# Optimization experiments

Measured on AMD Instinct MI355X. Metric: run time of the kernel, lower is better.

## Reference

```python
import jax, jax.numpy as jnp
import numpy as np

N, L, C, H = 8, 2048, 512, 512
C_HALF = max(C // 2, 1)


def setup_inputs() -> dict:
    key = jax.random.key(0)
    ks = jax.random.split(key, 11)
    s = 0.02
    return {
        "x": jax.random.normal(ks[0], (N, L, C), dtype=jnp.float32),
        "theta_w": jax.random.normal(ks[1], (C, H), dtype=jnp.float32) * s,
        "theta_b": jax.random.normal(ks[2], (H,), dtype=jnp.float32) * s,
        "phi_w": jax.random.normal(ks[3], (C, H), dtype=jnp.float32) * s,
        "phi_b": jax.random.normal(ks[4], (H,), dtype=jnp.float32) * s,
        "psi_w": jax.random.normal(ks[5], (C, H), dtype=jnp.float32) * s,
        "psi_b": jax.random.normal(ks[6], (H,), dtype=jnp.float32) * s,
        "r1_w": jax.random.normal(ks[7], (H, C_HALF), dtype=jnp.float32) * s,
        "r1_b": jax.random.normal(ks[8], (C_HALF,), dtype=jnp.float32) * s,
        "r2_w": jax.random.normal(ks[9], (C_HALF, C), dtype=jnp.float32) * s,
        "r2_b": jax.random.normal(ks[10], (C,), dtype=jnp.float32) * s,
    }


def reference(x, theta_w, theta_b, phi_w, phi_b, psi_w, psi_b, r1_w, r1_b, r2_w, r2_b):
    # projections: [n, L, h]
    x_t = x @ theta_w + theta_b
    x_ph = x @ phi_w + phi_b
    x_psi = x @ psi_w + psi_b
    # unscaled attention: phi @ theta^T -> [n, L, L], softmax over last dim
    attn = jax.nn.softmax(jnp.einsum("nlh,nmh->nlm", x_ph, x_t), axis=2)
    x_add = jnp.einsum("nlm,nmh->nlh", attn, x_psi)
    # recover MLP with LeakyReLU(0.2) then Tanh, residual add
    h1 = jax.nn.leaky_relu(x_add @ r1_w + r1_b, negative_slope=0.2)
    h2 = jnp.tanh(h1 @ r2_w + r2_b)
    return x + h2
```

## Files before the change

### kernel.cpp

```cpp
#include <hip/hip_runtime.h>
#include <hip/hip_bf16.h>

typedef float f32x4 __attribute__((ext_vector_type(4)));
typedef int   v8i   __attribute__((ext_vector_type(8)));
typedef __attribute__((address_space(3))) unsigned int       lds_uint;
typedef __attribute__((address_space(1))) const unsigned int glb_uint;

__device__ __forceinline__ float tanh_fast(float x) {
    float e = __expf(-2.0f * fabsf(x));
    float r = (1.0f - e) / (1.0f + e);
    return copysignf(r, x);
}
__device__ __forceinline__ unsigned char f2fp8(float v) {
    return (unsigned char)(__builtin_amdgcn_cvt_pk_fp8_f32(v, 0.0f, 0, false) & 0xff);
}
__device__ __forceinline__ unsigned short f2h(float v) {
    _Float16 h = (_Float16)v;
    unsigned short u;
    __builtin_memcpy(&u, &h, 2);
    return u;
}
__device__ __forceinline__ float h2f(unsigned short u) {
    _Float16 h;
    __builtin_memcpy(&h, &u, 2);
    return (float)h;
}

__global__ __launch_bounds__(256) void prep(
    const float* __restrict__ x,
    const float* __restrict__ theta_w, const float* __restrict__ phi_w,
    const float* __restrict__ psi_w,   const float* __restrict__ r1_w,
    const float* __restrict__ r2_w,
    const float* __restrict__ theta_b, const float* __restrict__ phi_b,
    const float* __restrict__ psi_b,
    unsigned char* __restrict__ xb8, unsigned char* __restrict__ wCat8T,
    unsigned char* __restrict__ r1T8, unsigned char* __restrict__ r2T8,
    float* __restrict__ bCat) {
    const int b = blockIdx.x, t = threadIdx.x;
    if (b < 8192) {
        long i = ((long)b * 256 + t) * 4;
        float4 f = *(const float4*)(x + i);
        int w = __builtin_amdgcn_cvt_pk_fp8_f32(f.x, f.y, 0, false);
        w = __builtin_amdgcn_cvt_pk_fp8_f32(f.z, f.w, w, true);
        *(unsigned int*)(xb8 + i) = (unsigned int)w;
    } else if (b < 11264) {
        const int sel = (b - 8192) >> 10;
        const int idx = ((b - 8192) & 1023) * 256 + t;
        const float* w = sel == 0 ? theta_w : (sel == 1 ? phi_w : psi_w);
        const int r = idx >> 9, c = idx & 511;
        wCat8T[(long)(sel * 512 + c) * 512 + r] = f2fp8(w[idx] * 16.0f);
    } else if (b < 11776) {
        const int idx = (b - 11264) * 256 + t;
        const int r = idx >> 8, c = idx & 255;
        r1T8[(long)c * 512 + r] = f2fp8(r1_w[idx] * 16.0f);
    } else if (b < 12288) {
        const int idx = (b - 11776) * 256 + t;
        const int r = idx >> 9, c = idx & 511;
        r2T8[(long)c * 256 + r] = f2fp8(r2_w[idx] * 16.0f);
    } else {
        const int i = (b - 12288) * 256 + t;
        if (i < 1536)
            bCat[i] = i < 512 ? theta_b[i] : (i < 1024 ? phi_b[i - 512] : psi_b[i - 1024]);
    }
}

__global__ __launch_bounds__(256) void softmax_fp8(unsigned short* __restrict__ S) {
    const size_t row = (size_t)blockIdx.y * 2048 + blockIdx.x;
    unsigned short* p = S + row * 2048;
    const int t = threadIdx.x;
    uint4 raw = *(uint4*)(p + t * 8);
    unsigned int w[4] = {raw.x, raw.y, raw.z, raw.w};
    float v[8];
#pragma unroll
    for (int i = 0; i < 4; ++i) {
        v[2 * i]     = h2f((unsigned short)(w[i] & 0xffffu));
        v[2 * i + 1] = h2f((unsigned short)(w[i] >> 16));
    }
    float mx = v[0];
#pragma unroll
    for (int i = 1; i < 8; ++i) mx = fmaxf(mx, v[i]);
#pragma unroll
    for (int off = 32; off > 0; off >>= 1) mx = fmaxf(mx, __shfl_xor(mx, off));
    __shared__ float red[8];
    const int wave = t >> 6, lane = t & 63;
    if (lane == 0) red[wave] = mx;
    __syncthreads();
    mx = fmaxf(fmaxf(red[0], red[1]), fmaxf(red[2], red[3]));
    float s = 0.0f;
#pragma unroll
    for (int i = 0; i < 8; ++i) { v[i] = __expf(v[i] - mx); s += v[i]; }
#pragma unroll
    for (int off = 32; off > 0; off >>= 1) s += __shfl_xor(s, off);
    if (lane == 0) red[4 + wave] = s;
    __syncthreads();
    s = red[4] + red[5] + red[6] + red[7];
    const float inv = 1.0f / s;
    int o0 = __builtin_amdgcn_cvt_pk_fp8_f32(v[0] * inv, v[1] * inv, 0, false);
    o0 = __builtin_amdgcn_cvt_pk_fp8_f32(v[2] * inv, v[3] * inv, o0, true);
    int o1 = __builtin_amdgcn_cvt_pk_fp8_f32(v[4] * inv, v[5] * inv, 0, false);
    o1 = __builtin_amdgcn_cvt_pk_fp8_f32(v[6] * inv, v[7] * inv, o1, true);
    uint2 ov; ov.x = (unsigned int)o0; ov.y = (unsigned int)o1;
    *(uint2*)((unsigned char*)p + t * 8) = ov;
}

template <int MODE>
__global__ __launch_bounds__(256) void gemm_fp8(
    const unsigned char* __restrict__ A,
    const unsigned char* __restrict__ Bt,
    const float* __restrict__ bias,
    const float* __restrict__ resid,
    unsigned char* __restrict__ out8,
    float* __restrict__ outF,
    int K, int ldaB, int ldbB, int ldc, long sA, long sB, long sC) {
    __shared__ unsigned char As[2][128 * 128];
    __shared__ unsigned char Bs[2][128 * 128];

    const int tid  = threadIdx.x;
    const int lane = tid & 63, wave = tid >> 6;
    const int m16  = lane & 15, quad = lane >> 4;
    const int wm   = (wave >> 1) << 6, wn = (wave & 1) << 6;
    const int m0   = blockIdx.x << 7, n0 = blockIdx.y << 7;

    const int srow = lane >> 3;
    const int uswz = (lane & 7) ^ srow;

    const unsigned char* Abase = A  + (long)blockIdx.z * sA + (long)m0 * ldaB;
    const unsigned char* Bbase = Bt + (long)blockIdx.z * sB + (long)n0 * ldbB;
    const int stR = (wave << 5) + srow;
    const long gA0 = (long)stR * ldaB + (uswz << 4);
    const long gB0 = (long)stR * ldbB + (uswz << 4);

    const int s8  = m16 & 7;
    const int P   = quad ^ (s8 >> 1);
    const int cLo = (P << 1) + (s8 & 1);
    const int offLo = cLo << 4;
    const int offHi = (cLo ^ 1) << 4;

    f32x4 acc[4][4] = {};
    union F8 { v8i v; int4 q[2]; };

    auto STAGE = [&](int buf, int kk) {
#pragma unroll
        for (int i = 0; i < 4; ++i) {
            const unsigned char* gp = Abase + gA0 + (long)(i << 3) * ldaB + kk;
            unsigned char* lp = &As[buf][((wave << 5) + (i << 3)) << 7];
            __builtin_amdgcn_global_load_lds((glb_uint*)gp, (lds_uint*)lp, 16, 0, 0);
        }
#pragma unroll
        for (int i = 0; i < 4; ++i) {
            const unsigned char* gp = Bbase + gB0 + (long)(i << 3) * ldbB + kk;
            unsigned char* lp = &Bs[buf][((wave << 5) + (i << 3)) << 7];
            __builtin_amdgcn_global_load_lds((glb_uint*)gp, (lds_uint*)lp, 16, 0, 0);
        }
    };

    STAGE(0, 0);
    int cur = 0;
    for (int k0 = 0; k0 < K; k0 += 128) {
        if (k0 + 128 < K) {
            STAGE(cur ^ 1, k0 + 128);
            asm volatile("s_waitcnt vmcnt(8)" ::: "memory");
        } else {
            asm volatile("s_waitcnt vmcnt(0)" ::: "memory");
        }
        asm volatile("s_barrier" ::: "memory");

        const unsigned char* Ab = As[cur];
        const unsigned char* Bb = Bs[cur];
        F8 af[4], bg[4];
#pragma unroll
        for (int f = 0; f < 4; ++f) {
            const int m = wm + (f << 4) + m16;
            const int n = wn + (f << 4) + m16;
            af[f].q[0] = *(const int4*)&Ab[(m << 7) + offLo];
            af[f].q[1] = *(const int4*)&Ab[(m << 7) + offHi];
            bg[f].q[0] = *(const int4*)&Bb[(n << 7) + offLo];
            bg[f].q[1] = *(const int4*)&Bb[(n << 7) + offHi];
        }
#pragma unroll
        for (int fi = 0; fi < 4; ++fi)
#pragma unroll
            for (int fj = 0; fj < 4; ++fj)
                acc[fi][fj] = __builtin_amdgcn_mfma_scale_f32_16x16x128_f8f6f4(
                    af[fi].v, bg[fj].v, acc[fi][fj],
                    0, 0, 0, 127, 0, 127);

        asm volatile("s_waitcnt lgkmcnt(0)" ::: "memory");
        asm volatile("s_barrier" ::: "memory");
        cur ^= 1;
    }

    const long zC = (long)blockIdx.z * sC;

#pragma unroll
    for (int fj = 0; fj < 4; ++fj) {
        const int col = n0 + wn + (fj << 4) + m16;
        float bv = 0.0f;
        if (MODE >= 3) bv = bias[col];
#pragma unroll
        for (int fi = 0; fi < 4; ++fi)
#pragma unroll
            for (int r = 0; r < 4; ++r) {
                const int row = m0 + wm + (fi << 4) + (quad << 2) + r;
                float v = acc[fi][fj][r];
                if (MODE == 2) {
                    out8[zC + (long)row * 512 + col] = f2fp8(v);
                } else if (MODE == 3) {
                    v = v * 0.0625f + bv;
                    v = v > 0.0f ? v : 0.2f * v;
                    out8[(long)row * 256 + col] = f2fp8(v);
                } else {
                    v = v * 0.0625f + bv;
                    const long idx = (long)row * ldc + col;
                    outF[idx] = tanh_fast(v) + resid[idx];
                }
            }
    }
}

template <int MODE>
__global__ __launch_bounds__(512, 2) void gemm_fp8_big(
    const unsigned char* __restrict__ A,
    const unsigned char* __restrict__ Bt,
    const float* __restrict__ bias,
    unsigned short* __restrict__ outH,
    unsigned char* __restrict__ out8,
    unsigned char* __restrict__ out8b,
    unsigned char* __restrict__ outV,
    int K, int ldaB, int ldbB, int ldc, long sA, long sB, long sC) {
    __shared__ unsigned char As[2][256 * 128];
    __shared__ unsigned char Bs[2][256 * 128];

    const int tid  = threadIdx.x;
    const int lane = tid & 63, wave = tid >> 6;
    const int m16  = lane & 15, quad = lane >> 4;
    const int wm   = (wave >> 2) << 7;
    const int wn   = (wave & 3) << 6;
    const int m0   = blockIdx.x << 8, n0 = blockIdx.y << 8;

    const int srow = lane >> 3;
    const int uswz = (lane & 7) ^ srow;

    const unsigned char* Abase = A  + (long)blockIdx.z * sA + (long)m0 * ldaB;
    const unsigned char* Bbase = Bt + (long)blockIdx.z * sB + (long)n0 * ldbB;
    const int stR = (wave << 5) + srow;
    const long gA0 = (long)stR * ldaB + (uswz << 4);
    const long gB0 = (long)stR * ldbB + (uswz << 4);

    const int s8  = m16 & 7;
    const int P   = quad ^ (s8 >> 1);
    const int cLo = (P << 1) + (s8 & 1);
    const int offLo = cLo << 4;
    const int offHi = (cLo ^ 1) << 4;

    f32x4 acc[8][4] = {};
    union F8 { v8i v; int4 q[2]; };

    auto STAGE = [&](int buf, int kk) {
#pragma unroll
        for (int i = 0; i < 4; ++i) {
            const unsigned char* gp = Abase + gA0 + (long)(i << 3) * ldaB + kk;
            unsigned char* lp = &As[buf][((wave << 5) + (i << 3)) << 7];
            __builtin_amdgcn_global_load_lds((glb_uint*)gp, (lds_uint*)lp, 16, 0, 0);
        }
#pragma unroll
        for (int i = 0; i < 4; ++i) {
            const unsigned char* gp = Bbase + gB0 + (long)(i << 3) * ldbB + kk;
            unsigned char* lp = &Bs[buf][((wave << 5) + (i << 3)) << 7];
            __builtin_amdgcn_global_load_lds((glb_uint*)gp, (lds_uint*)lp, 16, 0, 0);
        }
    };

    STAGE(0, 0);
    int cur = 0;
    for (int k0 = 0; k0 < K; k0 += 128) {
        if (k0 + 128 < K) {
            STAGE(cur ^ 1, k0 + 128);
            asm volatile("s_waitcnt vmcnt(8)" ::: "memory");
        } else {
            asm volatile("s_waitcnt vmcnt(0)" ::: "memory");
        }
        asm volatile("s_barrier" ::: "memory");

        const unsigned char* Ab = As[cur];
        const unsigned char* Bb = Bs[cur];
        F8 bg[4];
#pragma unroll
        for (int fj = 0; fj < 4; ++fj) {
            const int n = wn + (fj << 4) + m16;
            bg[fj].q[0] = *(const int4*)&Bb[(n << 7) + offLo];
            bg[fj].q[1] = *(const int4*)&Bb[(n << 7) + offHi];
        }
#pragma unroll
        for (int fi = 0; fi < 8; ++fi) {
            F8 af;
            const int m = wm + (fi << 4) + m16;
            af.q[0] = *(const int4*)&Ab[(m << 7) + offLo];
            af.q[1] = *(const int4*)&Ab[(m << 7) + offHi];
#pragma unroll
            for (int fj = 0; fj < 4; ++fj)
                acc[fi][fj] = __builtin_amdgcn_mfma_scale_f32_16x16x128_f8f6f4(
                    af.v, bg[fj].v, acc[fi][fj],
                    0, 0, 0, 127, 0, 127);
        }

        asm volatile("s_waitcnt lgkmcnt(0)" ::: "memory");
        asm volatile("s_barrier" ::: "memory");
        cur ^= 1;
    }

    const long zC = (long)blockIdx.z * sC;

    if (MODE == 0) {
        const int sel = n0 >> 9;
        if (sel < 2) {
            unsigned char* dst = sel == 0 ? out8 : out8b;
#pragma unroll
            for (int fj = 0; fj < 4; ++fj) {
                const int col = n0 + wn + (fj << 4) + m16;
                const int cb  = col & 511;
                const float bv = bias[col];
#pragma unroll
                for (int fi = 0; fi < 8; ++fi)
#pragma unroll
                    for (int r = 0; r < 4; ++r) {
                        const int row = m0 + wm + (fi << 4) + (quad << 2) + r;
                        dst[(long)row * 512 + cb] = f2fp8(acc[fi][fj][r] * 0.0625f + bv);
                    }
            }
        } else {
            const int z = m0 >> 11, l0 = (m0 & 2047) + wm + (quad << 2);
#pragma unroll
            for (int fj = 0; fj < 4; ++fj) {
                const int col = n0 + wn + (fj << 4) + m16;
                const int h   = col & 511;
                const float bv = bias[col];
#pragma unroll
                for (int fi = 0; fi < 8; ++fi) {
                    int w = __builtin_amdgcn_cvt_pk_fp8_f32(
                        acc[fi][fj][0] * 0.0625f + bv, acc[fi][fj][1] * 0.0625f + bv, 0, false);
                    w = __builtin_amdgcn_cvt_pk_fp8_f32(
                        acc[fi][fj][2] * 0.0625f + bv, acc[fi][fj][3] * 0.0625f + bv, w, true);
                    *(unsigned int*)(outV + ((long)z * 512 + h) * 2048 + l0 + (fi << 4)) =
                        (unsigned int)w;
                }
            }
        }
    } else {
#pragma unroll
        for (int fj = 0; fj < 4; ++fj) {
            const int col = n0 + wn + (fj << 4) + m16;
#pragma unroll
            for (int fi = 0; fi < 8; ++fi)
#pragma unroll
                for (int r = 0; r < 4; ++r) {
                    const int row = m0 + wm + (fi << 4) + (quad << 2) + r;
                    outH[zC + (long)row * ldc + col] = f2h(acc[fi][fj][r]);
                }
        }
    }
}

extern "C" void kernel_launch(void* const* d_in, const int* in_sizes, int n_in,
                              void* d_out, int out_size, void* d_ws, size_t ws_size,
                              hipStream_t stream) {
    const float* x       = (const float*)d_in[0];
    const float* theta_w = (const float*)d_in[1];
    const float* theta_b = (const float*)d_in[2];
    const float* phi_w   = (const float*)d_in[3];
    const float* phi_b   = (const float*)d_in[4];
    const float* psi_w   = (const float*)d_in[5];
    const float* psi_b   = (const float*)d_in[6];
    const float* r1_w    = (const float*)d_in[7];
    const float* r1_b    = (const float*)d_in[8];
    const float* r2_w    = (const float*)d_in[9];
    const float* r2_b    = (const float*)d_in[10];
    float* out = (float*)d_out;

    constexpr int  N = 8, L = 2048, C = 512, H = 512, CH = 256;
    constexpr long NL = (long)N * L;

    char* p = (char*)d_ws;
    auto alloc = [&](size_t bytes) { void* q = (void*)p; p += bytes; return q; };
    unsigned char*  xb8    = (unsigned char*)alloc(NL * C);
    unsigned char*  TH8    = (unsigned char*)alloc(NL * H);
    unsigned char*  PH8    = (unsigned char*)alloc(NL * H);
    unsigned char*  VT8    = (unsigned char*)alloc((long)N * H * L);
    unsigned char*  xadd8  = (unsigned char*)alloc(NL * H);
    unsigned char*  h18    = (unsigned char*)alloc(NL * CH);
    unsigned char*  wCat8T = (unsigned char*)alloc((long)1536 * 512);
    unsigned char*  r1T8   = (unsigned char*)alloc((long)H * CH);
    unsigned char*  r2T8   = (unsigned char*)alloc((long)CH * C);
    float*          bCat   = (float*)alloc(1536 * 4 + 256);
    unsigned short* S      = (unsigned short*)alloc((long)N * L * L * 2);

    prep<<<12294, 256, 0, stream>>>(x, theta_w, phi_w, psi_w, r1_w, r2_w,
                                    theta_b, phi_b, psi_b, xb8, wCat8T, r1T8, r2T8, bCat);

    gemm_fp8_big<0><<<dim3(NL / 256, 1536 / 256, 1), 512, 0, stream>>>(
        xb8, wCat8T, bCat, nullptr, TH8, PH8, VT8,
        C, C, C, 0, 0, 0, 0);

    gemm_fp8_big<1><<<dim3(L / 256, L / 256, N), 512, 0, stream>>>(
        PH8, TH8, nullptr, S, nullptr, nullptr, nullptr,
        H, H, H, L, (long)L * H, (long)L * H, (long)L * L);

    softmax_fp8<<<dim3(L, N), 256, 0, stream>>>(S);

    gemm_fp8<2><<<dim3(L / 128, H / 128, N), 256, 0, stream>>>(
        (const unsigned char*)S, VT8, nullptr, nullptr, xadd8, nullptr,
        L, 2 * L, L, H, (long)L * 2 * L, (long)H * L, (long)L * H);

    gemm_fp8<3><<<dim3(NL / 128, CH / 128, 1), 256, 0, stream>>>(
        xadd8, r1T8, r1_b, nullptr, h18, nullptr,
        H, H, H, CH, 0, 0, 0);

    gemm_fp8<4><<<dim3(NL / 128, C / 128, 1), 256, 0, stream>>>(
        h18, r2T8, r2_b, x, nullptr, out,
        CH, CH, CH, C, 0, 0, 0);
}
```

Baseline: 227.9 us.

## Rewrite 256-tile fp8 GEMM with quarter-staged prefetch and batch-interleaved block order

Replaces the big fp8 GEMM with a version that issues the next K-tile's loads in four quarters interleaved with four compute phases, each phase loading two A fragments, with barriers between phases and s_setprio raised around the MFMA groups. It also flattens the grid for the batched S and attention-V GEMMs so consecutive block IDs map to different batch indices, which changes how blocks are spread across XCDs and caches. Launch bounds drop the min-2-blocks hint. The goal is better overlap of global-to-LDS traffic with MFMA work. The cost is extra barriers per K-step and possibly more register pressure without the occupancy hint.

```diff
diff --git a/kernel.cpp b/kernel.cpp
--- a/kernel.cpp
+++ b/kernel.cpp
@@ -104,6 +104,161 @@
 }
 
 template <int MODE>
+__global__ __launch_bounds__(512) void gemm256(
+    const unsigned char* __restrict__ A,
+    const unsigned char* __restrict__ Bt,
+    const float* __restrict__ bias,
+    unsigned short* __restrict__ outH,
+    unsigned char* __restrict__ out8,
+    unsigned char* __restrict__ out8b,
+    unsigned char* __restrict__ outV,
+    int K, int ldaB, int ldbB, int ldc, long sA, long sB, long sC) {
+    __shared__ unsigned char As[2][256 * 128];
+    __shared__ unsigned char Bs[2][256 * 128];
+
+    const int tid  = threadIdx.x;
+    const int lane = tid & 63, wave = tid >> 6;
+    const int m16  = lane & 15, quad = lane >> 4;
+    const int wm   = (wave >> 2) << 7;
+    const int wn   = (wave & 3) << 6;
+
+    int bx, by, z;
+    if constexpr (MODE == 1) {
+        z = blockIdx.x & 7;
+        const int t = blockIdx.x >> 3;
+        by = t & 7; bx = t >> 3;
+    } else {
+        bx = blockIdx.x; by = blockIdx.y; z = 0;
+    }
+    const int m0 = bx << 8, n0 = by << 8;
+
+    const unsigned char* Abase = A  + (long)z * sA + (long)m0 * ldaB;
+    const unsigned char* Bbase = Bt + (long)z * sB + (long)n0 * ldbB;
+
+    const int s8  = m16 & 7;
+    const int P   = quad ^ (s8 >> 1);
+    const int cLo = (P << 1) + (s8 & 1);
+    const int offLo = cLo << 4;
+    const int offHi = (cLo ^ 1) << 4;
+
+    f32x4 acc[8][4] = {};
+    union F8 { v8i v; int4 q[2]; };
+
+    auto STAGEQ = [&](int buf, int kk, int q) {
+        const bool isA = !(q & 1);
+        const int  h   = q >> 1;
+        const unsigned char* gb = isA ? Abase : Bbase;
+        const long ld = isA ? (long)ldaB : (long)ldbB;
+        unsigned char* lb = isA ? As[buf] : Bs[buf];
+#pragma unroll
+        for (int i = 0; i < 2; ++i) {
+            const int slot = wave * 2 + i;
+            const int row  = h * 128 + slot * 8 + (lane >> 3);
+            const int su   = (lane & 7) ^ (row & 7);
+            __builtin_amdgcn_global_load_lds(
+                (glb_uint*)(gb + (long)row * ld + kk + (su << 4)),
+                (lds_uint*)(lb + h * 16384 + slot * 1024), 16, 0, 0);
+        }
+    };
+
+    const int KT = K >> 7;
+    STAGEQ(0, 0, 0); STAGEQ(0, 0, 1); STAGEQ(0, 0, 2); STAGEQ(0, 0, 3);
+
+    for (int t = 0; t < KT; ++t) {
+        const int  cb  = t & 1;
+        const int  kk1 = (t + 1) << 7;
+        const bool pf  = (t + 1 < KT);
+        F8 bg[4];
+#pragma unroll
+        for (int p = 0; p < 4; ++p) {
+            if (pf) STAGEQ(cb ^ 1, kk1, p);
+            if (p == 0) {
+                if (pf) asm volatile("s_waitcnt vmcnt(2)" ::: "memory");
+                else    asm volatile("s_waitcnt vmcnt(0)" ::: "memory");
+            }
+            asm volatile("s_barrier" ::: "memory");
+
+            F8 af[2];
+            if (p == 0) {
+#pragma unroll
+                for (int fj = 0; fj < 4; ++fj) {
+                    const int n = wn + (fj << 4) + m16;
+                    bg[fj].q[0] = *(const int4*)&Bs[cb][(n << 7) + offLo];
+                    bg[fj].q[1] = *(const int4*)&Bs[cb][(n << 7) + offHi];
+                }
+            }
+#pragma unroll
+            for (int e = 0; e < 2; ++e) {
+                const int m = wm + (((p << 1) + e) << 4) + m16;
+                af[e].q[0] = *(const int4*)&As[cb][(m << 7) + offLo];
+                af[e].q[1] = *(const int4*)&As[cb][(m << 7) + offHi];
+            }
+            asm volatile("s_waitcnt lgkmcnt(0)" ::: "memory");
+            __builtin_amdgcn_s_setprio(1);
+#pragma unroll
+            for (int e = 0; e < 2; ++e)
+#pragma unroll
+                for (int fj = 0; fj < 4; ++fj)
+                    acc[(p << 1) + e][fj] = __builtin_amdgcn_mfma_scale_f32_16x16x128_f8f6f4(
+                        af[e].v, bg[fj].v, acc[(p << 1) + e][fj], 0, 0, 0, 127, 0, 127);
+            __builtin_amdgcn_s_setprio(0);
+            asm volatile("s_barrier" ::: "memory");
+        }
+    }
+
+    if (MODE == 0) {
+        const int sel = n0 >> 9;
+        if (sel < 2) {
+            unsigned char* dst = sel == 0 ? out8 : out8b;
+#pragma unroll
+            for (int fj = 0; fj < 4; ++fj) {
+                const int col = n0 + wn + (fj << 4) + m16;
+                const int cb2 = col & 511;
+                const float bv = bias[col];
+#pragma unroll
+                for (int fi = 0; fi < 8; ++fi)
+#pragma unroll
+                    for (int r = 0; r < 4; ++r) {
+                        const int row = m0 + wm + (fi << 4) + (quad << 2) + r;
+                        dst[(long)row * 512 + cb2] = f2fp8(acc[fi][fj][r] * 0.0625f + bv);
+                    }
+            }
+        } else {
+            const int zz = m0 >> 11;
+#pragma unroll
+            for (int fj = 0; fj < 4; ++fj) {
+                const int col = n0 + wn + (fj << 4) + m16;
+                const int h   = col & 511;
+                const float bv = bias[col];
+#pragma unroll
+                for (int fi = 0; fi < 8; ++fi) {
+                    const int l0v = (m0 & 2047) + wm + (fi << 4) + (quad << 2);
+                    int w = __builtin_amdgcn_cvt_pk_fp8_f32(
+                        acc[fi][fj][0] * 0.0625f + bv, acc[fi][fj][1] * 0.0625f + bv, 0, false);
+                    w = __builtin_amdgcn_cvt_pk_fp8_f32(
+                        acc[fi][fj][2] * 0.0625f + bv, acc[fi][fj][3] * 0.0625f + bv, w, true);
+                    *(unsigned int*)(outV + ((long)zz * 512 + h) * 2048 + l0v) =
+                        (unsigned int)w;
+                }
+            }
+        }
+    } else {
+        const long zC = (long)z * sC;
+#pragma unroll
+        for (int fj = 0; fj < 4; ++fj) {
+            const int col = n0 + wn + (fj << 4) + m16;
+#pragma unroll
+            for (int fi = 0; fi < 8; ++fi)
+#pragma unroll
+                for (int r = 0; r < 4; ++r) {
+                    const int row = m0 + wm + (fi << 4) + (quad << 2) + r;
+                    outH[zC + (long)row * ldc + col] = f2h(acc[fi][fj][r]);
+                }
+        }
+    }
+}
+
+template <int MODE>
 __global__ __launch_bounds__(256) void gemm_fp8(
     const unsigned char* __restrict__ A,
     const unsigned char* __restrict__ Bt,
@@ -119,13 +274,22 @@
     const int lane = tid & 63, wave = tid >> 6;
     const int m16  = lane & 15, quad = lane >> 4;
     const int wm   = (wave >> 1) << 6, wn = (wave & 1) << 6;
-    const int m0   = blockIdx.x << 7, n0 = blockIdx.y << 7;
+
+    int bx, by, z;
+    if constexpr (MODE == 2) {
+        z = blockIdx.x & 7;
+        const int t = blockIdx.x >> 3;
+        by = t & 3;  bx = t >> 2;
+    } else {
+        bx = blockIdx.x; by = blockIdx.y; z = 0;
+    }
+    const int m0 = bx << 7, n0 = by << 7;
 
     const int srow = lane >> 3;
     const int uswz = (lane & 7) ^ srow;
 
-    const unsigned char* Abase = A  + (long)blockIdx.z * sA + (long)m0 * ldaB;
-    const unsigned char* Bbase = Bt + (long)blockIdx.z * sB + (long)n0 * ldbB;
+    const unsigned char* Abase = A  + (long)z * sA + (long)m0 * ldaB;
+    const unsigned char* Bbase = Bt + (long)z * sB + (long)n0 * ldbB;
     const int stR = (wave << 5) + srow;
     const long gA0 = (long)stR * ldaB + (uswz << 4);
     const long gB0 = (long)stR * ldbB + (uswz << 4);
@@ -190,7 +354,7 @@
         cur ^= 1;
     }
 
-    const long zC = (long)blockIdx.z * sC;
+    const long zC = (long)z * sC;
 
 #pragma unroll
     for (int fj = 0; fj < 4; ++fj) {
@@ -215,149 +379,6 @@
                     outF[idx] = tanh_fast(v) + resid[idx];
                 }
             }
-    }
-}
-
-template <int MODE>
-__global__ __launch_bounds__(512, 2) void gemm_fp8_big(
-    const unsigned char* __restrict__ A,
-    const unsigned char* __restrict__ Bt,
-    const float* __restrict__ bias,
-    unsigned short* __restrict__ outH,
-    unsigned char* __restrict__ out8,
-    unsigned char* __restrict__ out8b,
-    unsigned char* __restrict__ outV,
-    int K, int ldaB, int ldbB, int ldc, long sA, long sB, long sC) {
-    __shared__ unsigned char As[2][256 * 128];
-    __shared__ unsigned char Bs[2][256 * 128];
-
-    const int tid  = threadIdx.x;
-    const int lane = tid & 63, wave = tid >> 6;
-    const int m16  = lane & 15, quad = lane >> 4;
-    const int wm   = (wave >> 2) << 7;
-    const int wn   = (wave & 3) << 6;
-    const int m0   = blockIdx.x << 8, n0 = blockIdx.y << 8;
-
-    const int srow = lane >> 3;
-    const int uswz = (lane & 7) ^ srow;
-
-    const unsigned char* Abase = A  + (long)blockIdx.z * sA + (long)m0 * ldaB;
-    const unsigned char* Bbase = Bt + (long)blockIdx.z * sB + (long)n0 * ldbB;
-    const int stR = (wave << 5) + srow;
-    const long gA0 = (long)stR * ldaB + (uswz << 4);
-    const long gB0 = (long)stR * ldbB + (uswz << 4);
-
-    const int s8  = m16 & 7;
-    const int P   = quad ^ (s8 >> 1);
-    const int cLo = (P << 1) + (s8 & 1);
-    const int offLo = cLo << 4;
-    const int offHi = (cLo ^ 1) << 4;
-
-    f32x4 acc[8][4] = {};
-    union F8 { v8i v; int4 q[2]; };
-
-    auto STAGE = [&](int buf, int kk) {
-#pragma unroll
-        for (int i = 0; i < 4; ++i) {
-            const unsigned char* gp = Abase + gA0 + (long)(i << 3) * ldaB + kk;
-            unsigned char* lp = &As[buf][((wave << 5) + (i << 3)) << 7];
-            __builtin_amdgcn_global_load_lds((glb_uint*)gp, (lds_uint*)lp, 16, 0, 0);
-        }
-#pragma unroll
-        for (int i = 0; i < 4; ++i) {
-            const unsigned char* gp = Bbase + gB0 + (long)(i << 3) * ldbB + kk;
-            unsigned char* lp = &Bs[buf][((wave << 5) + (i << 3)) << 7];
-            __builtin_amdgcn_global_load_lds((glb_uint*)gp, (lds_uint*)lp, 16, 0, 0);
-        }
-    };
-
-    STAGE(0, 0);
-    int cur = 0;
-    for (int k0 = 0; k0 < K; k0 += 128) {
-        if (k0 + 128 < K) {
-            STAGE(cur ^ 1, k0 + 128);
-            asm volatile("s_waitcnt vmcnt(8)" ::: "memory");
-        } else {
-            asm volatile("s_waitcnt vmcnt(0)" ::: "memory");
-        }
-        asm volatile("s_barrier" ::: "memory");
-
-        const unsigned char* Ab = As[cur];
-        const unsigned char* Bb = Bs[cur];
-        F8 bg[4];
-#pragma unroll
-        for (int fj = 0; fj < 4; ++fj) {
-            const int n = wn + (fj << 4) + m16;
-            bg[fj].q[0] = *(const int4*)&Bb[(n << 7) + offLo];
-            bg[fj].q[1] = *(const int4*)&Bb[(n << 7) + offHi];
-        }
-#pragma unroll
-        for (int fi = 0; fi < 8; ++fi) {
-            F8 af;
-            const int m = wm + (fi << 4) + m16;
-            af.q[0] = *(const int4*)&Ab[(m << 7) + offLo];
-            af.q[1] = *(const int4*)&Ab[(m << 7) + offHi];
-#pragma unroll
-            for (int fj = 0; fj < 4; ++fj)
-                acc[fi][fj] = __builtin_amdgcn_mfma_scale_f32_16x16x128_f8f6f4(
-                    af.v, bg[fj].v, acc[fi][fj],
-                    0, 0, 0, 127, 0, 127);
-        }
-
-        asm volatile("s_waitcnt lgkmcnt(0)" ::: "memory");
-        asm volatile("s_barrier" ::: "memory");
-        cur ^= 1;
-    }
-
-    const long zC = (long)blockIdx.z * sC;
-
-    if (MODE == 0) {
-        const int sel = n0 >> 9;
-        if (sel < 2) {
-            unsigned char* dst = sel == 0 ? out8 : out8b;
-#pragma unroll
-            for (int fj = 0; fj < 4; ++fj) {
-                const int col = n0 + wn + (fj << 4) + m16;
-                const int cb  = col & 511;
-                const float bv = bias[col];
-#pragma unroll
-                for (int fi = 0; fi < 8; ++fi)
-#pragma unroll
-                    for (int r = 0; r < 4; ++r) {
-                        const int row = m0 + wm + (fi << 4) + (quad << 2) + r;
-                        dst[(long)row * 512 + cb] = f2fp8(acc[fi][fj][r] * 0.0625f + bv);
-                    }
-            }
-        } else {
-            const int z = m0 >> 11, l0 = (m0 & 2047) + wm + (quad << 2);
-#pragma unroll
-            for (int fj = 0; fj < 4; ++fj) {
-                const int col = n0 + wn + (fj << 4) + m16;
-                const int h   = col & 511;
-                const float bv = bias[col];
-#pragma unroll
-                for (int fi = 0; fi < 8; ++fi) {
-                    int w = __builtin_amdgcn_cvt_pk_fp8_f32(
-                        acc[fi][fj][0] * 0.0625f + bv, acc[fi][fj][1] * 0.0625f + bv, 0, false);
-                    w = __builtin_amdgcn_cvt_pk_fp8_f32(
-                        acc[fi][fj][2] * 0.0625f + bv, acc[fi][fj][3] * 0.0625f + bv, w, true);
-                    *(unsigned int*)(outV + ((long)z * 512 + h) * 2048 + l0 + (fi << 4)) =
-                        (unsigned int)w;
-                }
-            }
-        }
-    } else {
-#pragma unroll
-        for (int fj = 0; fj < 4; ++fj) {
-            const int col = n0 + wn + (fj << 4) + m16;
-#pragma unroll
-            for (int fi = 0; fi < 8; ++fi)
-#pragma unroll
-                for (int r = 0; r < 4; ++r) {
-                    const int row = m0 + wm + (fi << 4) + (quad << 2) + r;
-                    outH[zC + (long)row * ldc + col] = f2h(acc[fi][fj][r]);
-                }
-        }
     }
 }
 
@@ -397,17 +418,17 @@
     prep<<<12294, 256, 0, stream>>>(x, theta_w, phi_w, psi_w, r1_w, r2_w,
                                     theta_b, phi_b, psi_b, xb8, wCat8T, r1T8, r2T8, bCat);
 
-    gemm_fp8_big<0><<<dim3(NL / 256, 1536 / 256, 1), 512, 0, stream>>>(
+    gemm256<0><<<dim3(NL / 256, 1536 / 256, 1), 512, 0, stream>>>(
         xb8, wCat8T, bCat, nullptr, TH8, PH8, VT8,
         C, C, C, 0, 0, 0, 0);
 
-    gemm_fp8_big<1><<<dim3(L / 256, L / 256, N), 512, 0, stream>>>(
+    gemm256<1><<<dim3((L / 256) * (L / 256) * N, 1, 1), 512, 0, stream>>>(
         PH8, TH8, nullptr, S, nullptr, nullptr, nullptr,
         H, H, H, L, (long)L * H, (long)L * H, (long)L * L);
 
     softmax_fp8<<<dim3(L, N), 256, 0, stream>>>(S);
 
-    gemm_fp8<2><<<dim3(L / 128, H / 128, N), 256, 0, stream>>>(
+    gemm_fp8<2><<<dim3((L / 128) * (H / 128) * N, 1, 1), 256, 0, stream>>>(
         (const unsigned char*)S, VT8, nullptr, nullptr, xadd8, nullptr,
         L, 2 * L, L, H, (long)L * 2 * L, (long)H * L, (long)L * H);
 
```

Measured after the change: 236.5 us. 1.04x slower.
